# Optimization experiments

Hardware: AMD Instinct MI355X
Metric: run time of the kernel (lower is better)

Reference implementation:

```python
import jax, jax.numpy as jnp
import numpy as np

IN_DIM = 1024
HID = 256
OUT_DIM = 1000
NUM_BINS = 51
BATCH = 2048
N_LEGAL = 200


def setup_inputs() -> dict:
    key = jax.random.key(0)
    ks = jax.random.split(key, 12)
    s = lambda fan_in: 1.0 / np.sqrt(fan_in)
    u = lambda k, shp, b: jax.random.uniform(k, shp, jnp.float32, -b, b)
    return {
        "x": jax.random.normal(ks[0], (BATCH, IN_DIM), jnp.float32),
        # weights stored as [in, out] (math-equivalent to torch Linear)
        "w_in": u(ks[1], (IN_DIM, HID), s(IN_DIM)),
        "b_in": u(ks[2], (HID,), s(IN_DIM)),
        "w_ah": u(ks[3], (HID, HID), s(HID)),
        "b_ah": u(ks[4], (HID,), s(HID)),
        "w_ao": u(ks[5], (HID, OUT_DIM * NUM_BINS), s(HID)),
        "b_ao": u(ks[6], (OUT_DIM * NUM_BINS,), s(HID)),
        "w_vh": u(ks[7], (HID, HID), s(HID)),
        "b_vh": u(ks[8], (HID,), s(HID)),
        "w_vo": u(ks[9], (HID, NUM_BINS), s(HID)),
        "b_vo": u(ks[10], (NUM_BINS,), s(HID)),
        "v_range": jnp.linspace(-10.0, 10.0, NUM_BINS, dtype=jnp.float32),
        "possible_moves": jax.random.randint(ks[11], (BATCH, N_LEGAL), 0, OUT_DIM),
    }


def reference(x, w_in, b_in, w_ah, b_ah, w_ao, b_ao, w_vh, b_vh, w_vo, b_vo,
              v_range, possible_moves):
    B = x.shape[0]
    h = jax.nn.relu(x @ w_in + b_in)                       # [B, 256]
    adv_h = jax.nn.relu(h @ w_ah + b_ah)                   # [B, 256]
    val_h = jax.nn.relu(h @ w_vh + b_vh)                   # [B, 256]
    adv = (adv_h @ w_ao + b_ao).reshape(B, OUT_DIM, NUM_BINS)
    val = (val_h @ w_vo + b_vo).reshape(B, 1, NUM_BINS)
    q = val + adv - adv.mean(axis=1, keepdims=True)        # [B, A, bins]
    p = jnp.maximum(jax.nn.softmax(q, axis=2), 1e-5)       # softmax + clamp(min=1e-5)
    q_vals = jnp.sum(p * v_range, axis=2)                  # [B, A]
    # LegalSoftmax: per-row scatter of 1.0 at legal indices, vectorized
    mask = jnp.zeros((B, OUT_DIM), x.dtype).at[
        jnp.arange(B)[:, None], possible_moves].set(1.0)
    filtered = q_vals * mask
    # faithful to torch: any exact-zero entry (masked OR coincidental) -> -inf
    return jnp.where(filtered == 0, -jnp.inf, filtered)
```

## Files before the change

### kernel.cpp

```cpp
#include <hip/hip_runtime.h>
#include <cstdint>
#include <cstddef>

#define NB      2048
#define INDIM   1024
#define HID     256
#define NA      1000
#define BINS    51
#define NLEG    200
#define NPAIR   (NB*NLEG)
#define PPB     (NPAIR/256)
#define RSTRIDE 768
#define NSLICE  25

#define NEG_SENTINEL (-1.0e30f)

typedef float    f32x4  __attribute__((ext_vector_type(4)));
typedef __bf16   bf16x8 __attribute__((ext_vector_type(8)));
typedef unsigned short us8 __attribute__((ext_vector_type(8)));
typedef unsigned short us4 __attribute__((ext_vector_type(4)));
typedef unsigned long long u64x2 __attribute__((ext_vector_type(2)));

__device__ __forceinline__ unsigned short f2bf(float f) {
  union { float f; unsigned u; } v; v.f = f;
  return (unsigned short)((v.u + 0x7FFFu + ((v.u >> 16) & 1u)) >> 16);
}
__device__ __forceinline__ bf16x8 as_bf(us8 v) { return __builtin_bit_cast(bf16x8, v); }
__device__ __forceinline__ int imin(int a, int b) { return a < b ? a : b; }

__device__ __forceinline__ unsigned f2fp8x4(float a, float b, float c, float d) {
  int v = 0;
  v = __builtin_amdgcn_cvt_pk_fp8_f32(a, b, v, false);
  v = __builtin_amdgcn_cvt_pk_fp8_f32(c, d, v, true);
  return (unsigned)v;
}
__device__ __forceinline__ unsigned char f2fp8(float f) {
  int v = __builtin_amdgcn_cvt_pk_fp8_f32(f, 0.f, 0, false);
  return (unsigned char)(v & 0xff);
}
__device__ __forceinline__ float fp82f(unsigned char u) {
  return __builtin_amdgcn_cvt_f32_fp8((int)u, 0);
}

__global__ __launch_bounds__(256) void k_pre(
    const float* __restrict__ w_ao, unsigned char* __restrict__ wp8,
    float* __restrict__ wpart,
    const float* __restrict__ w_in, const float* __restrict__ w_ah,
    const float* __restrict__ w_vh,
    unsigned short* __restrict__ w_inT, unsigned short* __restrict__ w_ahT,
    unsigned short* __restrict__ w_vhT,
    float* __restrict__ out,
    const float* __restrict__ x, unsigned short* __restrict__ x_bf) {
  __shared__ __align__(16) unsigned char smem[16320];
  int b = blockIdx.x, tid = threadIdx.x;
  if (b < 1000) {
    unsigned char* st = smem;
    int s = b & 7, a0 = (b >> 3) * 8;
    const float* wbase = w_ao + (size_t)(s * 32) * (NA * BINS) + a0 * BINS;
    for (int i = tid; i < 816; i += 256) {
      int kq = i / 102, c4 = i - kq * 102;
      const float* rp = wbase + (size_t)(kq * 4) * (NA * BINS) + c4 * 4;
      float4 f0 = *(const float4*)(rp);
      float4 f1 = *(const float4*)(rp + NA * BINS);
      float4 f2 = *(const float4*)(rp + 2 * NA * BINS);
      float4 f3 = *(const float4*)(rp + 3 * NA * BINS);
      unsigned pk0 = f2fp8x4(f0.x * 16.f, f0.y * 16.f, f0.z * 16.f, f0.w * 16.f);
      unsigned pk1 = f2fp8x4(f1.x * 16.f, f1.y * 16.f, f1.z * 16.f, f1.w * 16.f);
      unsigned pk2 = f2fp8x4(f2.x * 16.f, f2.y * 16.f, f2.z * 16.f, f2.w * 16.f);
      unsigned pk3 = f2fp8x4(f3.x * 16.f, f3.y * 16.f, f3.z * 16.f, f3.w * 16.f);
      unsigned s01lo = __builtin_amdgcn_perm(pk1, pk0, 0x05010400u);
      unsigned s01hi = __builtin_amdgcn_perm(pk1, pk0, 0x07030602u);
      unsigned s23lo = __builtin_amdgcn_perm(pk3, pk2, 0x05010400u);
      unsigned s23hi = __builtin_amdgcn_perm(pk3, pk2, 0x07030602u);
      unsigned o0 = __builtin_amdgcn_perm(s23lo, s01lo, 0x05040100u);
      unsigned o1 = __builtin_amdgcn_perm(s23lo, s01lo, 0x07060302u);
      unsigned o2 = __builtin_amdgcn_perm(s23hi, s01hi, 0x05040100u);
      unsigned o3 = __builtin_amdgcn_perm(s23hi, s01hi, 0x07060302u);
      int k4 = kq * 4;
      int swz = ((c4 >> 2) & 3) << 3;
      int kb = ((k4 & 24) ^ swz) + (k4 & 7);
      int cbase = c4 * 160;
      *(unsigned*)(st + cbase + kb)       = o0;
      *(unsigned*)(st + cbase + 40 + kb)  = o1;
      *(unsigned*)(st + cbase + 80 + kb)  = o2;
      *(unsigned*)(st + cbase + 120 + kb) = o3;
    }
    __syncthreads();
    int slice = (b >> 3) % NSLICE;
    for (int i = tid; i < 32 * 51; i += 256) {
      int r = i / 51, j = i - r * 51;
      float s8 = 0.f;
#pragma unroll
      for (int aL = 0; aL < 8; aL++) {
        int c = aL * 51 + j;
        s8 += fp82f(st[c * 40 + ((r & 24) ^ (((c >> 4) & 3) << 3)) + (r & 7)]);
      }
      atomicAdd(&wpart[(size_t)slice * 13056 + (s * 32 + r) * 51 + j], s8);
    }
    int t4 = (tid >> 6) & 3, l = tid & 63;
    int col = t4 * 16 + (l & 15), kg = l >> 4;
    for (int aL = 0; aL < 8; aL++) {
      unsigned lo = 0, hi = 0;
      if (col < BINS) {
        int ci = aL * 51 + col;
        unsigned long long v8 = *(const unsigned long long*)(
            st + ci * 40 + ((kg * 8) ^ (((ci >> 4) & 3) << 3)));
        lo = (unsigned)v8; hi = (unsigned)(v8 >> 32);
      }
      uint2 v; v.x = lo; v.y = hi;
      *(uint2*)(wp8 + (size_t)(a0 + aL) * 16384 +
                (size_t)((s * 2 + (t4 >> 1)) * 64 + l) * 16 + (t4 & 1) * 8) = v;
    }
  } else if (b < 1384) {
    int bb = b - 1000;
    float (*tile)[33] = (float(*)[33])smem;
    const float* w; unsigned short* wT; int K, N, kt, nt;
    if (bb < 256)      { w = w_in; wT = w_inT; K = INDIM; N = HID; kt = bb & 31;        nt = bb >> 5; }
    else if (bb < 320) { w = w_ah; wT = w_ahT; K = HID;   N = HID; kt = (bb - 256) & 7; nt = (bb - 256) >> 3; }
    else               { w = w_vh; wT = w_vhT; K = HID;   N = HID; kt = (bb - 320) & 7; nt = (bb - 320) >> 3; }
    int k0 = kt * 32, n0 = nt * 32;
    int cr = tid >> 5, cc = tid & 31;
#pragma unroll
    for (int it = 0; it < 4; it++)
      tile[cr + it * 8][cc] = w[(size_t)(k0 + cr + it * 8) * N + n0 + cc];
    __syncthreads();
#pragma unroll
    for (int it = 0; it < 4; it++)
      wT[(size_t)(n0 + cr + it * 8) * K + k0 + cc] = f2bf(tile[cc][cr + it * 8]);
  } else if (b < 1884) {
    int base = (b - 1384) * 1024 + tid;
    float4 v = {NEG_SENTINEL, NEG_SENTINEL, NEG_SENTINEL, NEG_SENTINEL};
#pragma unroll
    for (int it = 0; it < 4; it++) ((float4*)out)[base + it * 256] = v;
  } else {
    int base4 = (b - 1884) * 1024 + tid;
#pragma unroll
    for (int it = 0; it < 4; it++) {
      float4 v = ((const float4*)x)[base4 + it * 256];
      us4 o;
      o[0] = f2bf(v.x); o[1] = f2bf(v.y); o[2] = f2bf(v.z); o[3] = f2bf(v.w);
      ((us4*)x_bf)[base4 + it * 256] = o;
    }
  }
}

__global__ __launch_bounds__(256) void k_mid(
    const unsigned short* __restrict__ x_bf, const unsigned short* __restrict__ w_inT,
    const float* __restrict__ b_in, unsigned short* __restrict__ h_bf,
    const float* __restrict__ w_vo, const float* __restrict__ wpart,
    const float* __restrict__ b_vo, const float* __restrict__ b_ao,
    unsigned short* __restrict__ Wc, float* __restrict__ bias_c) {
  __shared__ __align__(16) char smem[1024];
  int b = blockIdx.x, tid = threadIdx.x;
  if (b < 512) {
    int w = tid >> 6, l = tid & 63, la = l & 15, g = l >> 4;
    int idx = b * 4 + w;
    int m0 = (idx & 127) * 16, n0 = (idx >> 7) * 16;
    f32x4 acc = {0.f, 0.f, 0.f, 0.f};
    const us8* Bp = (const us8*)(w_inT + (size_t)(n0 + la) * INDIM) + g;
    const us8* Ap = (const us8*)(x_bf + (size_t)(m0 + la) * INDIM) + g;
#pragma unroll 8
    for (int s = 0; s < 32; s++)
      acc = __builtin_amdgcn_mfma_f32_16x16x32_bf16(as_bf(Ap[s * 4]), as_bf(Bp[s * 4]),
                                                    acc, 0, 0, 0);
    float bb = b_in[n0 + la];
#pragma unroll
    for (int r = 0; r < 4; r++) {
      float v = fmaxf(acc[r] + bb, 0.f);
      h_bf[(size_t)(m0 + g * 4 + r) * HID + n0 + la] = f2bf(v);
    }
  } else {
    float* sred = (float*)smem;
    int n = b - 512, t = tid;
    for (int k = t; k < 512; k += 256) {
      float v = 0.f;
      if (n < BINS) {
        if (k < 256) {
          v = w_vo[(size_t)k * BINS + n];
        } else {
          float ssum = 0.f;
#pragma unroll
          for (int sl = 0; sl < NSLICE; sl++)
            ssum += wpart[(size_t)sl * 13056 + (k - 256) * 51 + n];
          v = -(0.001f / 16.f) * ssum;
        }
      }
      Wc[(size_t)n * 512 + k] = f2bf(v);
    }
    float acc = 0.f;
    if (n < BINS)
      for (int a = t; a < NA; a += 256) acc += b_ao[(size_t)a * BINS + n];
    sred[t] = acc;
    __syncthreads();
    for (int d = 128; d > 0; d >>= 1) { if (t < d) sred[t] += sred[t + d]; __syncthreads(); }
    if (t == 0) bias_c[n] = (n < BINS) ? (b_vo[n] - 0.001f * sred[0]) : 0.f;
  }
}

__global__ __launch_bounds__(256) void k_heads(
    const unsigned short* __restrict__ h,
    const unsigned short* __restrict__ wA, const float* __restrict__ bA,
    const unsigned short* __restrict__ wV, const float* __restrict__ bV,
    const unsigned short* __restrict__ Wc, const float* __restrict__ bias_c,
    unsigned char* __restrict__ Aext8, float* __restrict__ cbuf_f,
    const int* __restrict__ pm, int* __restrict__ cursor, int* __restrict__ rows) {
  __shared__ __align__(16) char smem[16896];
  int b = blockIdx.x, tid = threadIdx.x;
  if (b < 128) {
    unsigned short* aL = (unsigned short*)smem;
    unsigned short* vL = (unsigned short*)smem + 16 * 264;
    int w = tid >> 6, l = tid & 63, la = l & 15, g = l >> 4;
    int m0 = b * 16;
    const us8* Ap = (const us8*)(h + (size_t)(m0 + la) * HID) + g;
    us8 aF[8];
#pragma unroll
    for (int s = 0; s < 8; s++) aF[s] = Ap[s * 4];
#pragma unroll
    for (int part = 0; part < 2; part++) {
      const unsigned short* BT = part ? wV : wA;
      const float* bias = part ? bV : bA;
      unsigned short* oL = part ? vL : aL;
#pragma unroll
      for (int nt = 0; nt < 4; nt++) {
        int n0 = w * 64 + nt * 16;
        f32x4 acc = {0.f, 0.f, 0.f, 0.f};
        const us8* Bp = (const us8*)(BT + (size_t)(n0 + la) * HID) + g;
#pragma unroll
        for (int s = 0; s < 8; s++)
          acc = __builtin_amdgcn_mfma_f32_16x16x32_bf16(as_bf(aF[s]), as_bf(Bp[s * 4]),
                                                        acc, 0, 0, 0);
        float bb = bias[n0 + la];
#pragma unroll
        for (int r = 0; r < 4; r++) {
          float v = fmaxf(acc[r] + bb, 0.f);
          oL[(g * 4 + r) * 264 + n0 + la] = f2bf(v);
          if (part == 0)
            Aext8[(size_t)(m0 + g * 4 + r) * HID + n0 + la] = f2fp8(v);
        }
      }
    }
    __syncthreads();
    int n0c = w * 16;
    f32x4 acc = {0.f, 0.f, 0.f, 0.f};
    const us8* Vp  = (const us8*)(vL + la * 264) + g;
    const us8* Ap2 = (const us8*)(aL + la * 264) + g;
    const us8* BpV = (const us8*)(Wc + (size_t)(n0c + la) * 512) + g;
    const us8* BpA = (const us8*)(Wc + (size_t)(n0c + la) * 512 + 256) + g;
#pragma unroll
    for (int s = 0; s < 8; s++)
      acc = __builtin_amdgcn_mfma_f32_16x16x32_bf16(as_bf(Vp[s * 4]), as_bf(BpV[s * 4]),
                                                    acc, 0, 0, 0);
#pragma unroll
    for (int s = 0; s < 8; s++)
      acc = __builtin_amdgcn_mfma_f32_16x16x32_bf16(as_bf(Ap2[s * 4]), as_bf(BpA[s * 4]),
                                                    acc, 0, 0, 0);
    float bb = bias_c[n0c + la];
#pragma unroll
    for (int r = 0; r < 4; r++)
      cbuf_f[(size_t)(m0 + g * 4 + r) * 64 + n0c + la] = acc[r] + bb;
  } else {
    int* lc = (int*)smem;
    int* lbase = (int*)(smem + 4096);
    int blk = b - 128, t = tid;
    for (int i = t; i < NA; i += 256) lc[i] = 0;
    __syncthreads();
    int pbase = blk * PPB;
    for (int i = t; i < PPB; i += 256) atomicAdd(&lc[pm[pbase + i]], 1);
    __syncthreads();
    for (int i = t; i < NA; i += 256) {
      int v = lc[i];
      lbase[i] = v ? atomicAdd(&cursor[i], v) : 0;
      lc[i] = 0;
    }
    __syncthreads();
    for (int i = t; i < PPB; i += 256) {
      int a = pm[pbase + i];
      int r = atomicAdd(&lc[a], 1);
      rows[(size_t)a * RSTRIDE + lbase[a] + r] = (pbase + i) / NLEG;
    }
  }
}

#define PREF(P, RA_) do {                                                      \
  rA##P = (RA_);                                                               \
  const long long* Ap_ = (const long long*)(Aext8 + (size_t)rA##P * HID) + g;  \
  a##P##0 = Ap_[0];  a##P##1 = Ap_[4];  a##P##2 = Ap_[8];  a##P##3 = Ap_[12];  \
  a##P##4 = Ap_[16]; a##P##5 = Ap_[20]; a##P##6 = Ap_[24]; a##P##7 = Ap_[28];  \
  const float4* cf_ = (const float4*)(cbuf_f + (size_t)rA##P * 64);            \
  cq##P##0 = cf_[g];     cq##P##1 = cf_[4 + g];                                \
  cq##P##2 = cf_[8 + g]; cq##P##3 = cf_[12 + g];                               \
} while (0)

#define MSTEP(P, S) do {                                                       \
  u64x2 b01_ = sBv[(S * 2) * 64 + l];                                          \
  u64x2 b23_ = sBv[(S * 2 + 1) * 64 + l];                                      \
  acc0_ = __builtin_amdgcn_mfma_f32_16x16x32_fp8_fp8(                          \
      (long long)b01_[0], a##P##S, acc0_, 0, 0, 0);                            \
  acc1_ = __builtin_amdgcn_mfma_f32_16x16x32_fp8_fp8(                          \
      (long long)b01_[1], a##P##S, acc1_, 0, 0, 0);                            \
  acc2_ = __builtin_amdgcn_mfma_f32_16x16x32_fp8_fp8(                          \
      (long long)b23_[0], a##P##S, acc2_, 0, 0, 0);                            \
  acc3_ = __builtin_amdgcn_mfma_f32_16x16x32_fp8_fp8(                          \
      (long long)b23_[1], a##P##S, acc3_, 0, 0, 0);                            \
} while (0)

#define COMP(P, TILE) do {                                                     \
  f32x4 acc0_ = {0.f,0.f,0.f,0.f}, acc1_ = {0.f,0.f,0.f,0.f};                  \
  f32x4 acc2_ = {0.f,0.f,0.f,0.f}, acc3_ = {0.f,0.f,0.f,0.f};                  \
  __builtin_amdgcn_s_setprio(1);                                               \
  MSTEP(P, 0); MSTEP(P, 1); MSTEP(P, 2); MSTEP(P, 3);                          \
  MSTEP(P, 4); MSTEP(P, 5); MSTEP(P, 6); MSTEP(P, 7);                          \
  __builtin_amdgcn_s_setprio(0);                                               \
  float S_ = 0.f;                                                              \
  f32x4 e0_, e1_, e2_, e3_;                                                    \
  _Pragma("unroll") for (int r_ = 0; r_ < 4; r_++) {                           \
    e0_[r_] = __expf(fmaf(acc0_[r_], 0.0625f, cq##P##0[r_] + bao0[r_])); S_ += e0_[r_]; \
    e1_[r_] = __expf(fmaf(acc1_[r_], 0.0625f, cq##P##1[r_] + bao1[r_])); S_ += e1_[r_]; \
    e2_[r_] = __expf(fmaf(acc2_[r_], 0.0625f, cq##P##2[r_] + bao2[r_])); S_ += e2_[r_]; \
    e3_[r_] = __expf(fmaf(acc3_[r_], 0.0625f, cq##P##3[r_] + bao3[r_])); S_ += e3_[r_]; \
  }                                                                            \
  S_ += __shfl_xor(S_, 16); S_ += __shfl_xor(S_, 32);                          \
  float inv_ = 1.f / S_, qv_ = 0.f;                                            \
  _Pragma("unroll") for (int r_ = 0; r_ < 4; r_++) {                           \
    int bin_ = g * 4 + r_;                                                     \
    qv_ = fmaf(fmaxf(e0_[r_] * inv_, 1e-5f), (float)bin_ * 0.4f - 10.f, qv_);  \
    qv_ = fmaf(fmaxf(e1_[r_] * inv_, 1e-5f), (float)(bin_ + 16) * 0.4f - 10.f, qv_); \
    qv_ = fmaf(fmaxf(e2_[r_] * inv_, 1e-5f), (float)(bin_ + 32) * 0.4f - 10.f, qv_); \
    if (bin_ + 48 < BINS)                                                      \
      qv_ = fmaf(fmaxf(e3_[r_] * inv_, 1e-5f), (float)(bin_ + 48) * 0.4f - 10.f, qv_); \
  }                                                                            \
  qv_ += __shfl_xor(qv_, 16); qv_ += __shfl_xor(qv_, 32);                      \
  int gi_ = (TILE) * 16 + la;                                                  \
  if (g == 0 && gi_ < count)                                                   \
    out[(size_t)rA##P * NA + a] = (qv_ == 0.f) ? NEG_SENTINEL : qv_;           \
} while (0)

__global__ __launch_bounds__(256) void k_main_mfma(
    const unsigned char* __restrict__ Aext8,
    const float* __restrict__ cbuf_f,
    const unsigned char* __restrict__ wp8,
    const float* __restrict__ b_ao,
    const int* __restrict__ cnt,
    const int* __restrict__ rows,
    float* __restrict__ out) {
  __shared__ __align__(16) long long sB8[2048];
  const u64x2* sBv = (const u64x2*)sB8;
  int bx = blockIdx.x;
  int a = (bx & 7) * 125 + (bx >> 3);
  int count = cnt[a];
  int ntiles = (count + 15) >> 4;
  if (count == 0 || (int)(blockIdx.y * 4) >= ntiles) return;
  int tid = threadIdx.x;
  int w = tid >> 6, l = tid & 63, la = l & 15, g = l >> 4;
  int base = a * RSTRIDE;
  int t0 = blockIdx.y * 4 + w;

  int rQ0 = rows[base + imin( t0       * 16 + la, count - 1)];
  int rQ1 = rows[base + imin((t0 +  8) * 16 + la, count - 1)];
  int rQ2 = rows[base + imin((t0 + 16) * 16 + la, count - 1)];
  int rQ3 = rows[base + imin((t0 + 24) * 16 + la, count - 1)];

  const float* baop = b_ao + (size_t)a * BINS;
  f32x4 bao0, bao1, bao2, bao3;
#pragma unroll
  for (int r = 0; r < 4; r++) {
    int bin = g * 4 + r;
    bao0[r] = baop[bin];
    bao1[r] = baop[bin + 16];
    bao2[r] = baop[bin + 32];
    bao3[r] = (bin + 48 < BINS) ? baop[bin + 48] : NEG_SENTINEL;
  }

  const u64x2* wpa = (const u64x2*)(wp8 + (size_t)a * 16384);
#pragma unroll
  for (int i = 0; i < 4; i++) ((u64x2*)sB8)[tid + i * 256] = wpa[tid + i * 256];
  __syncthreads();

  int rAA, rAB;
  long long aA0, aA1, aA2, aA3, aA4, aA5, aA6, aA7;
  long long aB0, aB1, aB2, aB3, aB4, aB5, aB6, aB7;
  float4 cqA0, cqA1, cqA2, cqA3;
  float4 cqB0, cqB1, cqB2, cqB3;
  bool e0 = t0 < ntiles, e1 = t0 + 8 < ntiles,
       e2 = t0 + 16 < ntiles, e3 = t0 + 24 < ntiles;

  if (e0) PREF(A, rQ0);
  if (e1) PREF(B, rQ1);
  if (e0) COMP(A, t0);
  if (e2) PREF(A, rQ2);
  if (e1) COMP(B, t0 + 8);
  if (e3) PREF(B, rQ3);
  if (e2) COMP(A, t0 + 16);
  if (e3) COMP(B, t0 + 24);
  for (int tile = t0 + 32; tile < ntiles; tile += 8) {
    int rAt = rows[base + imin(tile * 16 + la, count - 1)];
    PREF(A, rAt);
    COMP(A, tile);
  }
}

extern "C" void kernel_launch(void* const* d_in, const int* in_sizes, int n_in,
                              void* d_out, int out_size, void* d_ws, size_t ws_size,
                              hipStream_t stream) {
  (void)in_sizes; (void)n_in; (void)out_size; (void)ws_size;
  const float* x     = (const float*)d_in[0];
  const float* w_in  = (const float*)d_in[1];
  const float* b_in  = (const float*)d_in[2];
  const float* w_ah  = (const float*)d_in[3];
  const float* b_ah  = (const float*)d_in[4];
  const float* w_ao  = (const float*)d_in[5];
  const float* b_ao  = (const float*)d_in[6];
  const float* w_vh  = (const float*)d_in[7];
  const float* b_vh  = (const float*)d_in[8];
  const float* w_vo  = (const float*)d_in[9];
  const float* b_vo  = (const float*)d_in[10];
  const int*   pm    = (const int*)d_in[12];
  float* out = (float*)d_out;

  char* p = (char*)d_ws;
  unsigned char*  wp8    = (unsigned char*)p;  p += (size_t)NA * 32 * 512;
  unsigned char*  Aext8  = (unsigned char*)p;  p += (size_t)NB * HID;
  unsigned short* h_bf   = (unsigned short*)p; p += (size_t)NB * HID * 2;
  unsigned short* w_inT  = (unsigned short*)p; p += (size_t)HID * INDIM * 2;
  unsigned short* w_ahT  = (unsigned short*)p; p += (size_t)HID * HID * 2;
  unsigned short* w_vhT  = (unsigned short*)p; p += (size_t)HID * HID * 2;
  unsigned short* Wc     = (unsigned short*)p; p += (size_t)64 * 512 * 2;
  unsigned short* x_bf   = (unsigned short*)p; p += (size_t)NB * INDIM * 2;
  float* bias_c = (float*)p; p += 64 * 4;
  float* cbuf_f = (float*)p; p += (size_t)NB * 64 * 4;
  float* wpart  = (float*)p; p += (size_t)NSLICE * 13056 * 4;
  int* cursor = (int*)p; p += (size_t)NA * 4 + 240;
  int* rows   = (int*)p; p += (size_t)NA * RSTRIDE * 4 + 256;

  hipMemsetAsync(wpart, 0, ((size_t)NSLICE * 13056 + NA) * sizeof(float), stream);

  k_pre<<<2396, 256, 0, stream>>>(w_ao, wp8, wpart, w_in, w_ah, w_vh,
                                  w_inT, w_ahT, w_vhT, out, x, x_bf);
  k_mid<<<576, 256, 0, stream>>>(x_bf, w_inT, b_in, h_bf,
                                 w_vo, wpart, b_vo, b_ao, Wc, bias_c);
  k_heads<<<384, 256, 0, stream>>>(h_bf, w_ahT, b_ah, w_vhT, b_vh,
                                   Wc, bias_c, Aext8, cbuf_f,
                                   pm, cursor, rows);
  k_main_mfma<<<dim3(1000, 2), 256, 0, stream>>>(Aext8, cbuf_f, wp8, b_ao,
                                                 cursor, rows, out);
}
```

Baseline: 206.5 us.

## Collapse sliced atomic partial sums into single buffer and pin main-kernel schedule

Removes the 25-way slicing of the w_ao column-mean accumulator. All blocks now atomically add into one 13056-float buffer, which shrinks the memset and lets k_mid read one value instead of summing 25 slices. This raises atomic contention on each address (125 adders per element instead of about 5). Separately, sched_barrier pins are inserted between the prefetch and compute stages of k_main_mfma's prologue so the compiler cannot reorder them.

```diff
diff --git a/kernel.cpp b/kernel.cpp
--- a/kernel.cpp
+++ b/kernel.cpp
@@ -11,7 +11,6 @@
 #define NPAIR   (NB*NLEG)
 #define PPB     (NPAIR/256)
 #define RSTRIDE 768
-#define NSLICE  25
 
 #define NEG_SENTINEL (-1.0e30f)
 
@@ -44,7 +43,7 @@
 
 __global__ __launch_bounds__(256) void k_pre(
     const float* __restrict__ w_ao, unsigned char* __restrict__ wp8,
-    float* __restrict__ wpart,
+    float* __restrict__ wmean_acc,
     const float* __restrict__ w_in, const float* __restrict__ w_ah,
     const float* __restrict__ w_vh,
     unsigned short* __restrict__ w_inT, unsigned short* __restrict__ w_ahT,
@@ -86,7 +85,6 @@
       *(unsigned*)(st + cbase + 120 + kb) = o3;
     }
     __syncthreads();
-    int slice = (b >> 3) % NSLICE;
     for (int i = tid; i < 32 * 51; i += 256) {
       int r = i / 51, j = i - r * 51;
       float s8 = 0.f;
@@ -95,7 +93,7 @@
         int c = aL * 51 + j;
         s8 += fp82f(st[c * 40 + ((r & 24) ^ (((c >> 4) & 3) << 3)) + (r & 7)]);
       }
-      atomicAdd(&wpart[(size_t)slice * 13056 + (s * 32 + r) * 51 + j], s8);
+      atomicAdd(&wmean_acc[(size_t)(s * 32 + r) * BINS + j], s8);
     }
     int t4 = (tid >> 6) & 3, l = tid & 63;
     int col = t4 * 16 + (l & 15), kg = l >> 4;
@@ -147,7 +145,7 @@
 __global__ __launch_bounds__(256) void k_mid(
     const unsigned short* __restrict__ x_bf, const unsigned short* __restrict__ w_inT,
     const float* __restrict__ b_in, unsigned short* __restrict__ h_bf,
-    const float* __restrict__ w_vo, const float* __restrict__ wpart,
+    const float* __restrict__ w_vo, const float* __restrict__ wmean_acc,
     const float* __restrict__ b_vo, const float* __restrict__ b_ao,
     unsigned short* __restrict__ Wc, float* __restrict__ bias_c) {
   __shared__ __align__(16) char smem[1024];
@@ -174,17 +172,9 @@
     int n = b - 512, t = tid;
     for (int k = t; k < 512; k += 256) {
       float v = 0.f;
-      if (n < BINS) {
-        if (k < 256) {
-          v = w_vo[(size_t)k * BINS + n];
-        } else {
-          float ssum = 0.f;
-#pragma unroll
-          for (int sl = 0; sl < NSLICE; sl++)
-            ssum += wpart[(size_t)sl * 13056 + (k - 256) * 51 + n];
-          v = -(0.001f / 16.f) * ssum;
-        }
-      }
+      if (n < BINS)
+        v = (k < 256) ? w_vo[(size_t)k * BINS + n]
+                      : (-(0.001f / 16.f) * wmean_acc[(size_t)(k - 256) * BINS + n]);
       Wc[(size_t)n * 512 + k] = f2bf(v);
     }
     float acc = 0.f;
@@ -335,6 +325,8 @@
     out[(size_t)rA##P * NA + a] = (qv_ == 0.f) ? NEG_SENTINEL : qv_;           \
 } while (0)
 
+#define PIN() __builtin_amdgcn_sched_barrier(0)
+
 __global__ __launch_bounds__(256) void k_main_mfma(
     const unsigned char* __restrict__ Aext8,
     const float* __restrict__ cbuf_f,
@@ -386,10 +378,15 @@
 
   if (e0) PREF(A, rQ0);
   if (e1) PREF(B, rQ1);
+  PIN();
   if (e0) COMP(A, t0);
+  PIN();
   if (e2) PREF(A, rQ2);
+  PIN();
   if (e1) COMP(B, t0 + 8);
+  PIN();
   if (e3) PREF(B, rQ3);
+  PIN();
   if (e2) COMP(A, t0 + 16);
   if (e3) COMP(B, t0 + 24);
   for (int tile = t0 + 32; tile < ntiles; tile += 8) {
@@ -428,16 +425,16 @@
   unsigned short* x_bf   = (unsigned short*)p; p += (size_t)NB * INDIM * 2;
   float* bias_c = (float*)p; p += 64 * 4;
   float* cbuf_f = (float*)p; p += (size_t)NB * 64 * 4;
-  float* wpart  = (float*)p; p += (size_t)NSLICE * 13056 * 4;
+  float* wmean  = (float*)p; p += 13056 * 4;
   int* cursor = (int*)p; p += (size_t)NA * 4 + 240;
   int* rows   = (int*)p; p += (size_t)NA * RSTRIDE * 4 + 256;
 
-  hipMemsetAsync(wpart, 0, ((size_t)NSLICE * 13056 + NA) * sizeof(float), stream);
-
-  k_pre<<<2396, 256, 0, stream>>>(w_ao, wp8, wpart, w_in, w_ah, w_vh,
+  hipMemsetAsync(wmean, 0, (13056 + NA) * sizeof(float), stream);
+
+  k_pre<<<2396, 256, 0, stream>>>(w_ao, wp8, wmean, w_in, w_ah, w_vh,
                                   w_inT, w_ahT, w_vhT, out, x, x_bf);
   k_mid<<<576, 256, 0, stream>>>(x_bf, w_inT, b_in, h_bf,
-                                 w_vo, wpart, b_vo, b_ao, Wc, bias_c);
+                                 w_vo, wmean, b_vo, b_ao, Wc, bias_c);
   k_heads<<<384, 256, 0, stream>>>(h_bf, w_ahT, b_ah, w_vhT, b_vh,
                                    Wc, bias_c, Aext8, cbuf_f,
                                    pm, cursor, rows);
```

Measured after the change: 201.4 us. 1.03x faster.
